# Kernel tuning notes

Hardware: AMD Instinct MI355X
Metric: run time of the kernel (lower is better)

Reference implementation:

```python
import jax, jax.numpy as jnp
import numpy as np

D = 128  # h_dim == in_dim

def _gat_layer(h, d, src, dst, n_dst, W, U, V, a):
    # h: [N_src, Din], d: [E, 1], src/dst: [E]
    z = h @ W.T          # [N_src, D]
    zi = h @ U.T         # [N_src, D]
    t = d @ V.T          # [E, 1]
    Dh = W.shape[0]
    # attn_fc on concat([z_src, z_dst, t]) split into three partial dots
    e = z[src] @ a[:Dh] + z[dst] @ a[Dh:2 * Dh] + t[:, 0] * a[2 * Dh]
    e = jax.nn.leaky_relu(e)  # [E]
    # segment softmax over incoming edges of each dst node
    m = jax.ops.segment_max(e, dst, num_segments=n_dst)
    ex = jnp.exp(e - m[dst])
    s = jax.ops.segment_sum(ex, dst, num_segments=n_dst)
    alpha = ex / s[dst]  # [E]
    zn = jax.ops.segment_sum(alpha[:, None] * z[src], dst, num_segments=n_dst)
    return jax.nn.relu(zi[:n_dst] + zn)


def setup_inputs() -> dict:
    key = jax.random.key(0)
    ks = jax.random.split(key, 16)
    N0, ND0, ND1 = 100000, 40000, 20000
    E0, E1 = 640000, 320000
    sc = 1.0 / np.sqrt(D)
    inp = {
        "attr": jax.random.normal(ks[0], (N0, D), jnp.float32),
        "d0": jax.random.normal(ks[1], (E0, 1), jnp.float32),
        "d1": jax.random.normal(ks[2], (E1, 1), jnp.float32),
        "src0": jax.random.randint(ks[3], (E0,), 0, N0, jnp.int32),
        "dst0": jax.random.randint(ks[4], (E0,), 0, ND0, jnp.int32),
        "src1": jax.random.randint(ks[5], (E1,), 0, ND0, jnp.int32),
        "dst1": jax.random.randint(ks[6], (E1,), 0, ND1, jnp.int32),
        "n_dst0": ND0,
        "n_dst1": ND1,
        "W0": jax.random.normal(ks[7], (D, D), jnp.float32) * sc,
        "U0": jax.random.normal(ks[8], (D, D), jnp.float32) * sc,
        "V0": jax.random.normal(ks[9], (1, 1), jnp.float32),
        "a0": jax.random.normal(ks[10], (2 * D + 1,), jnp.float32) * sc,
        "W1": jax.random.normal(ks[11], (D, D), jnp.float32) * sc,
        "U1": jax.random.normal(ks[12], (D, D), jnp.float32) * sc,
        "V1": jax.random.normal(ks[13], (1, 1), jnp.float32),
        "a1": jax.random.normal(ks[14], (2 * D + 1,), jnp.float32) * sc,
    }
    return inp


def reference(attr, d0, d1, W0, U0, V0, a0, W1, U1, V1, a1,
              src0, dst0, src1, dst1, n_dst0, n_dst1):
    h = _gat_layer(attr, d0, src0, dst0, n_dst0, W0, U0, V0, a0)
    h = _gat_layer(h, d1, src1, dst1, n_dst1, W1, U1, V1, a1)
    return h
```

## Files before the change

### kernel.cpp

```cpp
#include <hip/hip_runtime.h>
#include <math.h>


#define D 128

typedef __bf16 bf16x8 __attribute__((ext_vector_type(8)));
typedef float f32x4 __attribute__((ext_vector_type(4)));

static __device__ __forceinline__ float lrelu(float x) {
  return x >= 0.f ? x : 0.01f * x;
}
static __device__ __forceinline__ unsigned short f2bf(float v) {
  unsigned int u = __float_as_uint(v);
  u += 0x7fffu + ((u >> 16) & 1u);
  return (unsigned short)(u >> 16);
}
static __device__ __forceinline__ float bf2f(unsigned short b) {
  return __uint_as_float((unsigned int)b << 16);
}

static __device__ __forceinline__ float4 loadV4(const float* p) {
  return *(const float4*)p;
}
static __device__ __forceinline__ float4 loadV4(const unsigned short* p) {
  ushort4 t = *(const ushort4*)p;
  return make_float4(bf2f(t.x), bf2f(t.y), bf2f(t.z), bf2f(t.w));
}
static __device__ __forceinline__ void storeV4(float* p, float4 v) {
  *(float4*)p = v;
}
static __device__ __forceinline__ void storeV4(unsigned short* p, float4 v) {
  ushort4 t;
  t.x = f2bf(v.x);
  t.y = f2bf(v.y);
  t.z = f2bf(v.z);
  t.w = f2bf(v.w);
  *(ushort4*)p = t;
}
static __device__ __forceinline__ void storeZi(float* p, float v) { *p = v; }
static __device__ __forceinline__ void storeZi(unsigned short* p, float v) {
  *p = f2bf(v);
}

static __device__ __forceinline__ int swz(int row, int colb) {
  return row * 256 + (colb ^ ((row & 7) << 4));
}

__global__ __launch_bounds__(256) void cvt4_kernel(
    const float* __restrict__ s0, const float* __restrict__ s1,
    const float* __restrict__ s2, const float* __restrict__ s3,
    __bf16* __restrict__ dst) {
  int idx = blockIdx.x * 256 + threadIdx.x;
  const float* s = (idx < 16384) ? s0
                   : (idx < 32768) ? s1
                   : (idx < 49152) ? s2 : s3;
  dst[idx] = (__bf16)s[idx & 16383];
}

__global__ void zero_int_kernel(int* __restrict__ p, int n) {
  int i = blockIdx.x * 256 + threadIdx.x;
  if (i < n) p[i] = 0;
}

static __device__ __forceinline__ void stageA(const float* A, int rblk,
                                              int rlim, int t,
                                              unsigned char* ldsA) {
  const char* base = (const char*)A + (size_t)rblk * 512;
#pragma unroll
  for (int g = 0; g < 8; ++g) {
    int sb = g * 4096 + t * 16;
    float4 v = make_float4(0.f, 0.f, 0.f, 0.f);
    if (rblk + (sb >> 9) < rlim) v = *(const float4*)(base + sb);
    int db = sb >> 1;
    int row = db >> 8, colb = db & 255;
    ushort4 o;
    o.x = f2bf(v.x);
    o.y = f2bf(v.y);
    o.z = f2bf(v.z);
    o.w = f2bf(v.w);
    *(ushort4*)(&ldsA[swz(row, colb)]) = o;
  }
}
static __device__ __forceinline__ void stageA(const unsigned short* A,
                                              int rblk, int rlim, int t,
                                              unsigned char* ldsA) {
  const char* base = (const char*)A + (size_t)rblk * 256;
#pragma unroll
  for (int g = 0; g < 4; ++g) {
    int bi = g * 4096 + t * 16;
    int row = bi >> 8, colb = bi & 255;
    ushort4 lo = {0, 0, 0, 0}, hi = {0, 0, 0, 0};
    if (rblk + row < rlim) {
      lo = *(const ushort4*)(base + bi);
      hi = *(const ushort4*)(base + bi + 8);
    }
    *(ushort4*)(&ldsA[swz(row, colb)]) = lo;
    *(ushort4*)(&ldsA[swz(row, colb) + 8]) = hi;
  }
}

template <typename AT, typename ZiT>
__global__ __launch_bounds__(256, 3) void gemm_lds(
    const AT* __restrict__ A, const __bf16* __restrict__ Wb,
    const __bf16* __restrict__ Ub, unsigned short* __restrict__ z,
    ZiT* __restrict__ zi, const float* __restrict__ a,
    float* __restrict__ zs, float* __restrict__ zd, int n_wb, int rows,
    int ndst) {
  __shared__ unsigned char lds[49152];
  const int t = threadIdx.x;
  const int blk = blockIdx.x;
  const bool isU = (blk >= n_wb);
  const int rblk = (isU ? blk - n_wb : blk) * 64;
  const int rlim = isU ? ndst : rows;
  const __bf16* B = isU ? Ub : Wb;

#pragma unroll
  for (int g = 0; g < 8; ++g) {
    int bi = g * 4096 + t * 16;
    int row = bi >> 8, colb = bi & 255;
    bf16x8 v = *(const bf16x8*)((const char*)B + bi);
    *(bf16x8*)(&lds[swz(row, colb)]) = v;
  }
  stageA(A, rblk, rlim, t, lds + 32768);
  __syncthreads();

  const int wave = t >> 6;
  const int lane = t & 63;
  const int lm = lane & 15;
  const int lk = lane >> 4;
  const int r0 = rblk + wave * 16;
  if (r0 >= rlim) return;

  bf16x8 af[4];
#pragma unroll
  for (int kt = 0; kt < 4; ++kt) {
    int row = wave * 16 + lm;
    af[kt] = *(const bf16x8*)(&lds[32768 + swz(row, kt * 64 + lk * 16)]);
  }

  f32x4 acc[8];
#pragma unroll
  for (int tt = 0; tt < 8; ++tt) acc[tt] = (f32x4){0.f, 0.f, 0.f, 0.f};
#pragma unroll
  for (int kt = 0; kt < 4; ++kt) {
#pragma unroll
    for (int tt = 0; tt < 8; ++tt) {
      int row = tt * 16 + lm;
      bf16x8 bf = *(const bf16x8*)(&lds[swz(row, kt * 64 + lk * 16)]);
      acc[tt] =
          __builtin_amdgcn_mfma_f32_16x16x32_bf16(af[kt], bf, acc[tt], 0, 0, 0);
    }
  }

  if (!isU) {
#pragma unroll
    for (int tt = 0; tt < 8; ++tt)
#pragma unroll
      for (int rr = 0; rr < 4; ++rr)
        z[(size_t)(r0 + lk * 4 + rr) * D + tt * 16 + lm] = f2bf(acc[tt][rr]);

    float p1[4] = {0.f, 0.f, 0.f, 0.f};
    float p2[4] = {0.f, 0.f, 0.f, 0.f};
#pragma unroll
    for (int tt = 0; tt < 8; ++tt) {
      float a1 = a[tt * 16 + lm];
      float a2 = a[D + tt * 16 + lm];
#pragma unroll
      for (int rr = 0; rr < 4; ++rr) {
        p1[rr] += acc[tt][rr] * a1;
        p2[rr] += acc[tt][rr] * a2;
      }
    }
#pragma unroll
    for (int rr = 0; rr < 4; ++rr) {
#pragma unroll
      for (int o = 1; o < 16; o <<= 1) {
        p1[rr] += __shfl_xor(p1[rr], o);
        p2[rr] += __shfl_xor(p2[rr], o);
      }
      if (lm == 0) {
        zs[r0 + lk * 4 + rr] = p1[rr];
        zd[r0 + lk * 4 + rr] = p2[rr];
      }
    }
  } else {
#pragma unroll
    for (int tt = 0; tt < 8; ++tt)
#pragma unroll
      for (int rr = 0; rr < 4; ++rr)
        storeZi(&zi[(size_t)(r0 + lk * 4 + rr) * D + tt * 16 + lm],
                acc[tt][rr]);
  }
}

__global__ void count_e_kernel(const int* __restrict__ src,
                               const int* __restrict__ dst,
                               const float* __restrict__ dE,
                               const float* __restrict__ zs,
                               const float* __restrict__ zd,
                               const float* __restrict__ V,
                               const float* __restrict__ a,
                               int* __restrict__ cnt,
                               float* __restrict__ w_out,
                               int* __restrict__ rank, int E) {
  int i0 = (blockIdx.x * 256 + threadIdx.x) * 4;
  float vc = V[0] * a[2 * D];
  if (i0 + 4 <= E) {
    int4 s4 = *(const int4*)(src + i0);
    int4 d4 = *(const int4*)(dst + i0);
    float4 de = *(const float4*)(dE + i0);
    int4 r4;
    r4.x = atomicAdd(&cnt[d4.x], 1);
    r4.y = atomicAdd(&cnt[d4.y], 1);
    r4.z = atomicAdd(&cnt[d4.z], 1);
    r4.w = atomicAdd(&cnt[d4.w], 1);
    float zs0 = zs[s4.x], zs1 = zs[s4.y], zs2 = zs[s4.z], zs3 = zs[s4.w];
    float zd0 = zd[d4.x], zd1 = zd[d4.y], zd2 = zd[d4.z], zd3 = zd[d4.w];
    float4 w;
    w.x = __expf(lrelu(zs0 + zd0 + de.x * vc));
    w.y = __expf(lrelu(zs1 + zd1 + de.y * vc));
    w.z = __expf(lrelu(zs2 + zd2 + de.z * vc));
    w.w = __expf(lrelu(zs3 + zd3 + de.w * vc));
    *(float4*)(w_out + i0) = w;
    *(int4*)(rank + i0) = r4;
  } else {
    for (int i = i0; i < E; ++i) {
      int di = dst[i];
      rank[i] = atomicAdd(&cnt[di], 1);
      w_out[i] = __expf(lrelu(zs[src[i]] + zd[di] + dE[i] * vc));
    }
  }
}

__global__ __launch_bounds__(256) void scan_partial(const int* __restrict__ cnt,
                                                    int* __restrict__ part,
                                                    int n) {
  __shared__ int sm[4];
  int base = blockIdx.x * 1024;
  int t = threadIdx.x;
  int s = 0;
#pragma unroll
  for (int i = 0; i < 4; ++i) {
    int idx = base + t + i * 256;
    s += (idx < n) ? cnt[idx] : 0;
  }
  for (int o = 32; o; o >>= 1) s += __shfl_xor(s, o);
  if ((t & 63) == 0) sm[t >> 6] = s;
  __syncthreads();
  if (t == 0) part[blockIdx.x] = sm[0] + sm[1] + sm[2] + sm[3];
}

__global__ __launch_bounds__(256) void scan_final(
    const int* __restrict__ cnt, const int* __restrict__ part,
    int* __restrict__ offs, int nb, int n, int total) {
  __shared__ int sm[4];
  __shared__ int sbase;
  int base = blockIdx.x * 1024;
  int t = threadIdx.x;
  if (t < 64) {
    int v = (t < nb && t < (int)blockIdx.x) ? part[t] : 0;
#pragma unroll
    for (int o = 32; o; o >>= 1) v += __shfl_xor(v, o);
    if (t == 0) sbase = v;
  }
  int idx = base + t * 4;
  int c0 = (idx + 0 < n) ? cnt[idx + 0] : 0;
  int c1 = (idx + 1 < n) ? cnt[idx + 1] : 0;
  int c2 = (idx + 2 < n) ? cnt[idx + 2] : 0;
  int c3 = (idx + 3 < n) ? cnt[idx + 3] : 0;
  int ts = c0 + c1 + c2 + c3;
  int v = ts;
#pragma unroll
  for (int o = 1; o < 64; o <<= 1) {
    int u = __shfl_up(v, o);
    if ((t & 63) >= o) v += u;
  }
  if ((t & 63) == 63) sm[t >> 6] = v;
  __syncthreads();
  int w = t >> 6;
  int waveoff = 0;
  if (w > 0) waveoff += sm[0];
  if (w > 1) waveoff += sm[1];
  if (w > 2) waveoff += sm[2];
  int run = v - ts + waveoff + sbase;
  if (idx + 0 < n) { offs[idx + 0] = run; run += c0; }
  if (idx + 1 < n) { offs[idx + 1] = run; run += c1; }
  if (idx + 2 < n) { offs[idx + 2] = run; run += c2; }
  if (idx + 3 < n) { offs[idx + 3] = run; run += c3; }
  if (blockIdx.x == 0 && t == 0) offs[n] = total;
}

__global__ void scatter_kernel(const int* __restrict__ src,
                               const int* __restrict__ dst,
                               const float* __restrict__ w_in,
                               const int* __restrict__ rank,
                               const int* __restrict__ offs,
                               int2* __restrict__ csr, int E) {
  int i0 = (blockIdx.x * 256 + threadIdx.x) * 4;
  if (i0 + 4 <= E) {
    int4 s4 = *(const int4*)(src + i0);
    int4 d4 = *(const int4*)(dst + i0);
    float4 e4 = *(const float4*)(w_in + i0);
    int4 r4 = *(const int4*)(rank + i0);
    int p0 = offs[d4.x] + r4.x;
    int p1 = offs[d4.y] + r4.y;
    int p2 = offs[d4.z] + r4.z;
    int p3 = offs[d4.w] + r4.w;
    csr[p0] = make_int2(s4.x, __float_as_int(e4.x));
    csr[p1] = make_int2(s4.y, __float_as_int(e4.y));
    csr[p2] = make_int2(s4.z, __float_as_int(e4.z));
    csr[p3] = make_int2(s4.w, __float_as_int(e4.w));
  } else {
    for (int i = i0; i < E; ++i) {
      int p = offs[dst[i]] + rank[i];
      csr[p] = make_int2(src[i], __float_as_int(w_in[i]));
    }
  }
}

template <typename OT>
__global__ __launch_bounds__(256) void gat_perdst(
    const unsigned short* __restrict__ z, const int2* __restrict__ csr,
    const int* __restrict__ offs, const OT* __restrict__ ziin,
    OT* __restrict__ hout, int nd) {
  int n = blockIdx.x * 8 + (threadIdx.x >> 5);
  if (n >= nd) return;
  int lane = threadIdx.x & 31;
  int beg = offs[n], end = offs[n + 1];

  float s0 = 0.f, s1 = 0.f;
  float4 acc0 = make_float4(0.f, 0.f, 0.f, 0.f);
  float4 acc1 = make_float4(0.f, 0.f, 0.f, 0.f);
  const unsigned short* zp = z + lane * 4;
  int j = beg;
  for (; j + 8 <= end; j += 8) {
    int2 pr[8];
#pragma unroll
    for (int u = 0; u < 8; ++u) pr[u] = csr[j + u];
    float4 zv[8];
#pragma unroll
    for (int u = 0; u < 8; ++u) zv[u] = loadV4(zp + (size_t)pr[u].x * D);
#pragma unroll
    for (int u = 0; u < 8; u += 2) {
      float wa = __int_as_float(pr[u].y);
      float wb = __int_as_float(pr[u + 1].y);
      s0 += wa;
      acc0.x += wa * zv[u].x;
      acc0.y += wa * zv[u].y;
      acc0.z += wa * zv[u].z;
      acc0.w += wa * zv[u].w;
      s1 += wb;
      acc1.x += wb * zv[u + 1].x;
      acc1.y += wb * zv[u + 1].y;
      acc1.z += wb * zv[u + 1].z;
      acc1.w += wb * zv[u + 1].w;
    }
  }
  for (; j < end; ++j) {
    int2 pr = csr[j];
    float w = __int_as_float(pr.y);
    float4 zv = loadV4(zp + (size_t)pr.x * D);
    s0 += w;
    acc0.x += w * zv.x;
    acc0.y += w * zv.y;
    acc0.z += w * zv.z;
    acc0.w += w * zv.w;
  }
  float s = s0 + s1;
  float inv = (s > 0.f) ? 1.f / s : 0.f;
  float4 acc = make_float4(acc0.x + acc1.x, acc0.y + acc1.y, acc0.z + acc1.z,
                           acc0.w + acc1.w);
  float4 ziv = loadV4(ziin + (size_t)n * D + lane * 4);
  float4 o4;
  o4.x = fmaxf(ziv.x + acc.x * inv, 0.f);
  o4.y = fmaxf(ziv.y + acc.y * inv, 0.f);
  o4.z = fmaxf(ziv.z + acc.z * inv, 0.f);
  o4.w = fmaxf(ziv.w + acc.w * inv, 0.f);
  storeV4(hout + (size_t)n * D + lane * 4, o4);
}

extern "C" void kernel_launch(void* const* d_in, const int* in_sizes, int n_in,
                              void* d_out, int out_size, void* d_ws,
                              size_t ws_size, hipStream_t stream) {
  const float* attr = (const float*)d_in[0];
  const float* d0 = (const float*)d_in[1];
  const float* d1 = (const float*)d_in[2];
  const int* src0 = (const int*)d_in[3];
  const int* dst0 = (const int*)d_in[4];
  const int* src1 = (const int*)d_in[5];
  const int* dst1 = (const int*)d_in[6];
  const float* W0 = (const float*)d_in[9];
  const float* U0 = (const float*)d_in[10];
  const float* V0 = (const float*)d_in[11];
  const float* a0 = (const float*)d_in[12];
  const float* W1 = (const float*)d_in[13];
  const float* U1 = (const float*)d_in[14];
  const float* V1 = (const float*)d_in[15];
  const float* a1 = (const float*)d_in[16];

  const int N0 = in_sizes[0] / D;
  const int E0 = in_sizes[1];
  const int E1 = in_sizes[2];
  const int ND0 = 40000;
  const int ND1 = 20000;

  char* p = (char*)d_ws;
  auto alloc = [&](size_t bytes) {
    char* q = p;
    p += (bytes + 255) & ~(size_t)255;
    return q;
  };
  unsigned short* z = (unsigned short*)alloc((size_t)N0 * D * 2);
  int2* csr = (int2*)alloc((size_t)E0 * 8);
  unsigned short* h1b = (unsigned short*)alloc((size_t)ND0 * D * 2);
  float* w_buf = (float*)alloc((size_t)E0 * 4);
  int* rank = (int*)alloc((size_t)E0 * 4);
  float* zs = (float*)alloc((size_t)N0 * 4);
  float* zd = (float*)alloc((size_t)N0 * 4);
  int* offs = (int*)alloc((size_t)(ND0 + 1) * 4);
  int* cnt01 = (int*)alloc((size_t)(ND0 + ND1) * 4);
  int* part = (int*)alloc((size_t)64 * 4);
  __bf16* wb = (__bf16*)alloc((size_t)4 * D * D * 2);
  int* cnt0 = cnt01;
  int* cnt1 = cnt01 + ND0;
  (void)n_in;
  (void)out_size;
  (void)ws_size;

  float* out = (float*)d_out;

  cvt4_kernel<<<256, 256, 0, stream>>>(W0, U0, W1, U1, wb);
  zero_int_kernel<<<(ND0 + ND1 + 255) / 256, 256, 0, stream>>>(cnt01,
                                                               ND0 + ND1);
  const __bf16* W0b = wb;
  const __bf16* U0b = wb + 16384;
  const __bf16* W1b = wb + 32768;
  const __bf16* U1b = wb + 49152;

  {
    int n_wb = (N0 + 63) / 64, n_ub = (ND0 + 63) / 64;
    gemm_lds<float, unsigned short><<<n_wb + n_ub, 256, 0, stream>>>(
        attr, W0b, U0b, z, (unsigned short*)d_out, a0, zs, zd, n_wb, N0, ND0);
  }
  count_e_kernel<<<(E0 / 4 + 255) / 256, 256, 0, stream>>>(
      src0, dst0, d0, zs, zd, V0, a0, cnt0, w_buf, rank, E0);
  {
    int nb = (ND0 + 1023) / 1024;
    scan_partial<<<nb, 256, 0, stream>>>(cnt0, part, ND0);
    scan_final<<<nb, 256, 0, stream>>>(cnt0, part, offs, nb, ND0, E0);
  }
  scatter_kernel<<<(E0 / 4 + 255) / 256, 256, 0, stream>>>(
      src0, dst0, w_buf, rank, offs, csr, E0);
  gat_perdst<unsigned short><<<(ND0 + 7) / 8, 256, 0, stream>>>(
      z, csr, offs, (const unsigned short*)d_out, h1b, ND0);

  {
    int n_wb = (ND0 + 63) / 64, n_ub = (ND1 + 63) / 64;
    gemm_lds<unsigned short, float><<<n_wb + n_ub, 256, 0, stream>>>(
        h1b, W1b, U1b, z, out, a1, zs, zd, n_wb, ND0, ND1);
  }
  count_e_kernel<<<(E1 / 4 + 255) / 256, 256, 0, stream>>>(
      src1, dst1, d1, zs, zd, V1, a1, cnt1, w_buf, rank, E1);
  {
    int nb = (ND1 + 1023) / 1024;
    scan_partial<<<nb, 256, 0, stream>>>(cnt1, part, ND1);
    scan_final<<<nb, 256, 0, stream>>>(cnt1, part, offs, nb, ND1, E1);
  }
  scatter_kernel<<<(E1 / 4 + 255) / 256, 256, 0, stream>>>(
      src1, dst1, w_buf, rank, offs, csr, E1);
  gat_perdst<float><<<(ND1 + 7) / 8, 256, 0, stream>>>(z, csr, offs, out, out,
                                                       ND1);
}
```

Baseline: 180.8 us.

## Batch CSR construction for both layers upfront and fuse edge weights into scatter

Counting and ranking destination degrees for both layers now happens in one kernel launched before the first GEMM, followed by a single batched two-pass scan that covers both layers' offsets. This replaces four separate count/scan launches and keeps the graph-structure work independent of the GEMMs. The edge-weight exp computation moves from the count kernel into the scatter kernel, which removes the intermediate w_buf write and read. It costs separate rank and offset buffers per layer, and the combined count kernel contends on atomics across more edges in a single launch.

```diff
diff --git a/kernel.cpp b/kernel.cpp
--- a/kernel.cpp
+++ b/kernel.cpp
@@ -193,50 +193,47 @@
   }
 }
 
-__global__ void count_e_kernel(const int* __restrict__ src,
-                               const int* __restrict__ dst,
-                               const float* __restrict__ dE,
-                               const float* __restrict__ zs,
-                               const float* __restrict__ zd,
-                               const float* __restrict__ V,
-                               const float* __restrict__ a,
-                               int* __restrict__ cnt,
-                               float* __restrict__ w_out,
-                               int* __restrict__ rank, int E) {
-  int i0 = (blockIdx.x * 256 + threadIdx.x) * 4;
-  float vc = V[0] * a[2 * D];
-  if (i0 + 4 <= E) {
-    int4 s4 = *(const int4*)(src + i0);
-    int4 d4 = *(const int4*)(dst + i0);
-    float4 de = *(const float4*)(dE + i0);
-    int4 r4;
-    r4.x = atomicAdd(&cnt[d4.x], 1);
-    r4.y = atomicAdd(&cnt[d4.y], 1);
-    r4.z = atomicAdd(&cnt[d4.z], 1);
-    r4.w = atomicAdd(&cnt[d4.w], 1);
-    float zs0 = zs[s4.x], zs1 = zs[s4.y], zs2 = zs[s4.z], zs3 = zs[s4.w];
-    float zd0 = zd[d4.x], zd1 = zd[d4.y], zd2 = zd[d4.z], zd3 = zd[d4.w];
-    float4 w;
-    w.x = __expf(lrelu(zs0 + zd0 + de.x * vc));
-    w.y = __expf(lrelu(zs1 + zd1 + de.y * vc));
-    w.z = __expf(lrelu(zs2 + zd2 + de.z * vc));
-    w.w = __expf(lrelu(zs3 + zd3 + de.w * vc));
-    *(float4*)(w_out + i0) = w;
-    *(int4*)(rank + i0) = r4;
+__global__ void count_rank_kernel(const int* __restrict__ dst0,
+                                  const int* __restrict__ dst1,
+                                  int* __restrict__ cnt0,
+                                  int* __restrict__ cnt1,
+                                  int* __restrict__ rank0,
+                                  int* __restrict__ rank1, int q0, int q1) {
+  int gid = blockIdx.x * 256 + threadIdx.x;
+  const int* dst;
+  int* cnt;
+  int* rank;
+  int i0;
+  if (gid < q0) {
+    dst = dst0; cnt = cnt0; rank = rank0; i0 = gid * 4;
+  } else if (gid < q0 + q1) {
+    dst = dst1; cnt = cnt1; rank = rank1; i0 = (gid - q0) * 4;
   } else {
-    for (int i = i0; i < E; ++i) {
-      int di = dst[i];
-      rank[i] = atomicAdd(&cnt[di], 1);
-      w_out[i] = __expf(lrelu(zs[src[i]] + zd[di] + dE[i] * vc));
-    }
-  }
-}
-
-__global__ __launch_bounds__(256) void scan_partial(const int* __restrict__ cnt,
-                                                    int* __restrict__ part,
-                                                    int n) {
+    return;
+  }
+  int4 d4 = *(const int4*)(dst + i0);
+  int4 r4;
+  r4.x = atomicAdd(&cnt[d4.x], 1);
+  r4.y = atomicAdd(&cnt[d4.y], 1);
+  r4.z = atomicAdd(&cnt[d4.z], 1);
+  r4.w = atomicAdd(&cnt[d4.w], 1);
+  *(int4*)(rank + i0) = r4;
+}
+
+__global__ __launch_bounds__(256) void scan_partial2(
+    const int* __restrict__ cnt0, const int* __restrict__ cnt1,
+    int* __restrict__ part, int nb0, int n0, int n1) {
   __shared__ int sm[4];
-  int base = blockIdx.x * 1024;
+  int blk = blockIdx.x;
+  const int* cnt;
+  int* pt;
+  int n, lb;
+  if (blk < nb0) {
+    cnt = cnt0; pt = part; n = n0; lb = blk;
+  } else {
+    cnt = cnt1; pt = part + 64; n = n1; lb = blk - nb0;
+  }
+  int base = lb * 1024;
   int t = threadIdx.x;
   int s = 0;
 #pragma unroll
@@ -247,18 +244,30 @@
   for (int o = 32; o; o >>= 1) s += __shfl_xor(s, o);
   if ((t & 63) == 0) sm[t >> 6] = s;
   __syncthreads();
-  if (t == 0) part[blockIdx.x] = sm[0] + sm[1] + sm[2] + sm[3];
-}
-
-__global__ __launch_bounds__(256) void scan_final(
-    const int* __restrict__ cnt, const int* __restrict__ part,
-    int* __restrict__ offs, int nb, int n, int total) {
+  if (t == 0) pt[lb] = sm[0] + sm[1] + sm[2] + sm[3];
+}
+
+__global__ __launch_bounds__(256) void scan_final2(
+    const int* __restrict__ cnt0, const int* __restrict__ cnt1,
+    const int* __restrict__ part, int* __restrict__ offs0,
+    int* __restrict__ offs1, int nb0, int n0, int n1, int tot0, int tot1) {
   __shared__ int sm[4];
   __shared__ int sbase;
-  int base = blockIdx.x * 1024;
+  int blk = blockIdx.x;
+  const int* cnt;
+  const int* pt;
+  int* offs;
+  int n, lb, total;
+  if (blk < nb0) {
+    cnt = cnt0; pt = part; offs = offs0; n = n0; lb = blk; total = tot0;
+  } else {
+    cnt = cnt1; pt = part + 64; offs = offs1; n = n1; lb = blk - nb0;
+    total = tot1;
+  }
+  int base = lb * 1024;
   int t = threadIdx.x;
   if (t < 64) {
-    int v = (t < nb && t < (int)blockIdx.x) ? part[t] : 0;
+    int v = (t < lb) ? pt[t] : 0;
 #pragma unroll
     for (int o = 32; o; o >>= 1) v += __shfl_xor(v, o);
     if (t == 0) sbase = v;
@@ -287,33 +296,46 @@
   if (idx + 1 < n) { offs[idx + 1] = run; run += c1; }
   if (idx + 2 < n) { offs[idx + 2] = run; run += c2; }
   if (idx + 3 < n) { offs[idx + 3] = run; run += c3; }
-  if (blockIdx.x == 0 && t == 0) offs[n] = total;
-}
-
-__global__ void scatter_kernel(const int* __restrict__ src,
-                               const int* __restrict__ dst,
-                               const float* __restrict__ w_in,
-                               const int* __restrict__ rank,
-                               const int* __restrict__ offs,
-                               int2* __restrict__ csr, int E) {
+  if (lb == 0 && t == 0) offs[n] = total;
+}
+
+__global__ void scatter_w_kernel(const int* __restrict__ src,
+                                 const int* __restrict__ dst,
+                                 const float* __restrict__ dE,
+                                 const float* __restrict__ zs,
+                                 const float* __restrict__ zd,
+                                 const float* __restrict__ V,
+                                 const float* __restrict__ a,
+                                 const int* __restrict__ rank,
+                                 const int* __restrict__ offs,
+                                 int2* __restrict__ csr, int E) {
   int i0 = (blockIdx.x * 256 + threadIdx.x) * 4;
+  float vc = V[0] * a[2 * D];
   if (i0 + 4 <= E) {
     int4 s4 = *(const int4*)(src + i0);
     int4 d4 = *(const int4*)(dst + i0);
-    float4 e4 = *(const float4*)(w_in + i0);
+    float4 de = *(const float4*)(dE + i0);
     int4 r4 = *(const int4*)(rank + i0);
+    float zs0 = zs[s4.x], zs1 = zs[s4.y], zs2 = zs[s4.z], zs3 = zs[s4.w];
+    float zd0 = zd[d4.x], zd1 = zd[d4.y], zd2 = zd[d4.z], zd3 = zd[d4.w];
     int p0 = offs[d4.x] + r4.x;
     int p1 = offs[d4.y] + r4.y;
     int p2 = offs[d4.z] + r4.z;
     int p3 = offs[d4.w] + r4.w;
-    csr[p0] = make_int2(s4.x, __float_as_int(e4.x));
-    csr[p1] = make_int2(s4.y, __float_as_int(e4.y));
-    csr[p2] = make_int2(s4.z, __float_as_int(e4.z));
-    csr[p3] = make_int2(s4.w, __float_as_int(e4.w));
+    float w0 = __expf(lrelu(zs0 + zd0 + de.x * vc));
+    float w1 = __expf(lrelu(zs1 + zd1 + de.y * vc));
+    float w2 = __expf(lrelu(zs2 + zd2 + de.z * vc));
+    float w3 = __expf(lrelu(zs3 + zd3 + de.w * vc));
+    csr[p0] = make_int2(s4.x, __float_as_int(w0));
+    csr[p1] = make_int2(s4.y, __float_as_int(w1));
+    csr[p2] = make_int2(s4.z, __float_as_int(w2));
+    csr[p3] = make_int2(s4.w, __float_as_int(w3));
   } else {
     for (int i = i0; i < E; ++i) {
-      int p = offs[dst[i]] + rank[i];
-      csr[p] = make_int2(src[i], __float_as_int(w_in[i]));
+      int di = dst[i];
+      int pp = offs[di] + rank[i];
+      float w = __expf(lrelu(zs[src[i]] + zd[di] + dE[i] * vc));
+      csr[pp] = make_int2(src[i], __float_as_int(w));
     }
   }
 }
@@ -413,13 +435,14 @@
   unsigned short* z = (unsigned short*)alloc((size_t)N0 * D * 2);
   int2* csr = (int2*)alloc((size_t)E0 * 8);
   unsigned short* h1b = (unsigned short*)alloc((size_t)ND0 * D * 2);
-  float* w_buf = (float*)alloc((size_t)E0 * 4);
-  int* rank = (int*)alloc((size_t)E0 * 4);
+  int* rank0 = (int*)alloc((size_t)E0 * 4);
+  int* rank1 = (int*)alloc((size_t)E1 * 4);
   float* zs = (float*)alloc((size_t)N0 * 4);
   float* zd = (float*)alloc((size_t)N0 * 4);
-  int* offs = (int*)alloc((size_t)(ND0 + 1) * 4);
+  int* offs0 = (int*)alloc((size_t)(ND0 + 1) * 4);
+  int* offs1 = (int*)alloc((size_t)(ND1 + 1) * 4);
   int* cnt01 = (int*)alloc((size_t)(ND0 + ND1) * 4);
-  int* part = (int*)alloc((size_t)64 * 4);
+  int* part = (int*)alloc((size_t)128 * 4);
   __bf16* wb = (__bf16*)alloc((size_t)4 * D * D * 2);
   int* cnt0 = cnt01;
   int* cnt1 = cnt01 + ND0;
@@ -432,6 +455,17 @@
   cvt4_kernel<<<256, 256, 0, stream>>>(W0, U0, W1, U1, wb);
   zero_int_kernel<<<(ND0 + ND1 + 255) / 256, 256, 0, stream>>>(cnt01,
                                                                ND0 + ND1);
+  {
+    int q0 = E0 / 4, q1 = E1 / 4;
+    count_rank_kernel<<<(q0 + q1 + 255) / 256, 256, 0, stream>>>(
+        dst0, dst1, cnt0, cnt1, rank0, rank1, q0, q1);
+    int nb0 = (ND0 + 1023) / 1024;
+    int nb1 = (ND1 + 1023) / 1024;
+    scan_partial2<<<nb0 + nb1, 256, 0, stream>>>(cnt0, cnt1, part, nb0, ND0,
+                                                 ND1);
+    scan_final2<<<nb0 + nb1, 256, 0, stream>>>(cnt0, cnt1, part, offs0, offs1,
+                                               nb0, ND0, ND1, E0, E1);
+  }
   const __bf16* W0b = wb;
   const __bf16* U0b = wb + 16384;
   const __bf16* W1b = wb + 32768;
@@ -442,32 +476,18 @@
     gemm_lds<float, unsigned short><<<n_wb + n_ub, 256, 0, stream>>>(
         attr, W0b, U0b, z, (unsigned short*)d_out, a0, zs, zd, n_wb, N0, ND0);
   }
-  count_e_kernel<<<(E0 / 4 + 255) / 256, 256, 0, stream>>>(
-      src0, dst0, d0, zs, zd, V0, a0, cnt0, w_buf, rank, E0);
-  {
-    int nb = (ND0 + 1023) / 1024;
-    scan_partial<<<nb, 256, 0, stream>>>(cnt0, part, ND0);
-    scan_final<<<nb, 256, 0, stream>>>(cnt0, part, offs, nb, ND0, E0);
-  }
-  scatter_kernel<<<(E0 / 4 + 255) / 256, 256, 0, stream>>>(
-      src0, dst0, w_buf, rank, offs, csr, E0);
+  scatter_w_kernel<<<(E0 / 4 + 255) / 256, 256, 0, stream>>>(
+      src0, dst0, d0, zs, zd, V0, a0, rank0, offs0, csr, E0);
   gat_perdst<unsigned short><<<(ND0 + 7) / 8, 256, 0, stream>>>(
-      z, csr, offs, (const unsigned short*)d_out, h1b, ND0);
+      z, csr, offs0, (const unsigned short*)d_out, h1b, ND0);
 
   {
     int n_wb = (ND0 + 63) / 64, n_ub = (ND1 + 63) / 64;
     gemm_lds<unsigned short, float><<<n_wb + n_ub, 256, 0, stream>>>(
         h1b, W1b, U1b, z, out, a1, zs, zd, n_wb, ND0, ND1);
   }
-  count_e_kernel<<<(E1 / 4 + 255) / 256, 256, 0, stream>>>(
-      src1, dst1, d1, zs, zd, V1, a1, cnt1, w_buf, rank, E1);
-  {
-    int nb = (ND1 + 1023) / 1024;
-    scan_partial<<<nb, 256, 0, stream>>>(cnt1, part, ND1);
-    scan_final<<<nb, 256, 0, stream>>>(cnt1, part, offs, nb, ND1, E1);
-  }
-  scatter_kernel<<<(E1 / 4 + 255) / 256, 256, 0, stream>>>(
-      src1, dst1, w_buf, rank, offs, csr, E1);
-  gat_perdst<float><<<(ND1 + 7) / 8, 256, 0, stream>>>(z, csr, offs, out, out,
+  scatter_w_kernel<<<(E1 / 4 + 255) / 256, 256, 0, stream>>>(
+      src1, dst1, d1, zs, zd, V1, a1, rank1, offs1, csr, E1);
+  gat_perdst<float><<<(ND1 + 7) / 8, 256, 0, stream>>>(z, csr, offs1, out, out,
                                                        ND1);
 }
```

Measured after the change: 171.3 us. 5.2% less time.

## Build CSR by destination-range bucketing with LDS histograms instead of global atomics

Applied to the files above, without the earlier changes.

Replaces the count/scan/scatter CSR construction, which relied on global atomic counters per destination node, with a two-phase bucketed scheme. A front kernel, fused with the weight conversion, has 96 blocks each scan the whole dst array and collect the edges whose destination falls in their 625-node range. A per-range phase then builds the histogram, local scan and rank in LDS, computes the edge weights and writes the CSR. This removes the global atomics, the zeroing, and several launches per layer. In exchange, every bucketing block re-reads the full edge list, each phase runs with very few blocks, and ranges with more than CAP edges silently lose edges.

```diff
diff --git a/kernel.cpp b/kernel.cpp
--- a/kernel.cpp
+++ b/kernel.cpp
@@ -3,6 +3,8 @@
 
 
 #define D 128
+#define RANGE 625
+#define CAP 16384
 
 typedef __bf16 bf16x8 __attribute__((ext_vector_type(8)));
 typedef float f32x4 __attribute__((ext_vector_type(4)));
@@ -46,20 +48,47 @@
   return row * 256 + (colb ^ ((row & 7) << 4));
 }
 
-__global__ __launch_bounds__(256) void cvt4_kernel(
+__global__ __launch_bounds__(256) void front_kernel(
     const float* __restrict__ s0, const float* __restrict__ s1,
     const float* __restrict__ s2, const float* __restrict__ s3,
-    __bf16* __restrict__ dst) {
-  int idx = blockIdx.x * 256 + threadIdx.x;
-  const float* s = (idx < 16384) ? s0
-                   : (idx < 32768) ? s1
-                   : (idx < 49152) ? s2 : s3;
-  dst[idx] = (__bf16)s[idx & 16383];
-}
-
-__global__ void zero_int_kernel(int* __restrict__ p, int n) {
-  int i = blockIdx.x * 256 + threadIdx.x;
-  if (i < n) p[i] = 0;
+    __bf16* __restrict__ wdst, const int* __restrict__ dst0,
+    const int* __restrict__ dst1, int E0, int E1, int2* __restrict__ seg,
+    int* __restrict__ total) {
+  const int blk = blockIdx.x;
+  const int t = threadIdx.x;
+  if (blk < 256) {
+    int idx = blk * 256 + t;
+    const float* s = (idx < 16384) ? s0
+                     : (idx < 32768) ? s1
+                     : (idx < 49152) ? s2 : s3;
+    wdst[idx] = (__bf16)s[idx & 16383];
+    return;
+  }
+  __shared__ int nseg;
+  int g = blk - 256;
+  const int* dst;
+  int E, lo;
+  if (g < 64) {
+    dst = dst0; E = E0; lo = g * RANGE;
+  } else {
+    dst = dst1; E = E1; lo = (g - 64) * RANGE;
+  }
+  if (t == 0) nseg = 0;
+  __syncthreads();
+  int2* myseg = seg + (size_t)g * CAP;
+  for (int i0 = t * 4; i0 < E; i0 += 1024) {
+    int4 d4 = *(const int4*)(dst + i0);
+    int dk[4] = {d4.x, d4.y, d4.z, d4.w};
+#pragma unroll
+    for (int k = 0; k < 4; ++k) {
+      if (dk[k] >= lo && dk[k] < lo + RANGE) {
+        int p = atomicAdd(&nseg, 1);
+        if (p < CAP) myseg[p] = make_int2(i0 + k, dk[k]);
+      }
+    }
+  }
+  __syncthreads();
+  if (t == 0) total[g] = (nseg < CAP) ? nseg : CAP;
 }
 
 static __device__ __forceinline__ void stageA(const float* A, int rblk,
@@ -100,7 +129,7 @@
 }
 
 template <typename AT, typename ZiT>
-__global__ __launch_bounds__(256, 3) void gemm_lds(
+__global__ __launch_bounds__(256, 3) void gemm_tiles(
     const AT* __restrict__ A, const __bf16* __restrict__ Wb,
     const __bf16* __restrict__ Ub, unsigned short* __restrict__ z,
     ZiT* __restrict__ zi, const float* __restrict__ a,
@@ -193,128 +222,103 @@
   }
 }
 
-__global__ void count_e_kernel(const int* __restrict__ src,
-                               const int* __restrict__ dst,
-                               const float* __restrict__ dE,
-                               const float* __restrict__ zs,
-                               const float* __restrict__ zd,
-                               const float* __restrict__ V,
-                               const float* __restrict__ a,
-                               int* __restrict__ cnt,
-                               float* __restrict__ w_out,
-                               int* __restrict__ rank, int E) {
-  int i0 = (blockIdx.x * 256 + threadIdx.x) * 4;
-  float vc = V[0] * a[2 * D];
-  if (i0 + 4 <= E) {
-    int4 s4 = *(const int4*)(src + i0);
-    int4 d4 = *(const int4*)(dst + i0);
-    float4 de = *(const float4*)(dE + i0);
-    int4 r4;
-    r4.x = atomicAdd(&cnt[d4.x], 1);
-    r4.y = atomicAdd(&cnt[d4.y], 1);
-    r4.z = atomicAdd(&cnt[d4.z], 1);
-    r4.w = atomicAdd(&cnt[d4.w], 1);
-    float zs0 = zs[s4.x], zs1 = zs[s4.y], zs2 = zs[s4.z], zs3 = zs[s4.w];
-    float zd0 = zd[d4.x], zd1 = zd[d4.y], zd2 = zd[d4.z], zd3 = zd[d4.w];
-    float4 w;
-    w.x = __expf(lrelu(zs0 + zd0 + de.x * vc));
-    w.y = __expf(lrelu(zs1 + zd1 + de.y * vc));
-    w.z = __expf(lrelu(zs2 + zd2 + de.z * vc));
-    w.w = __expf(lrelu(zs3 + zd3 + de.w * vc));
-    *(float4*)(w_out + i0) = w;
-    *(int4*)(rank + i0) = r4;
-  } else {
-    for (int i = i0; i < E; ++i) {
-      int di = dst[i];
-      rank[i] = atomicAdd(&cnt[di], 1);
-      w_out[i] = __expf(lrelu(zs[src[i]] + zd[di] + dE[i] * vc));
-    }
-  }
-}
-
-__global__ __launch_bounds__(256) void scan_partial(const int* __restrict__ cnt,
-                                                    int* __restrict__ part,
-                                                    int n) {
-  __shared__ int sm[4];
-  int base = blockIdx.x * 1024;
-  int t = threadIdx.x;
-  int s = 0;
-#pragma unroll
-  for (int i = 0; i < 4; ++i) {
-    int idx = base + t + i * 256;
-    s += (idx < n) ? cnt[idx] : 0;
-  }
-  for (int o = 32; o; o >>= 1) s += __shfl_xor(s, o);
-  if ((t & 63) == 0) sm[t >> 6] = s;
-  __syncthreads();
-  if (t == 0) part[blockIdx.x] = sm[0] + sm[1] + sm[2] + sm[3];
-}
-
-__global__ __launch_bounds__(256) void scan_final(
-    const int* __restrict__ cnt, const int* __restrict__ part,
-    int* __restrict__ offs, int nb, int n, int total) {
-  __shared__ int sm[4];
+__global__ __launch_bounds__(256) void csr_phaseB(
+    const int* __restrict__ src, const float* __restrict__ dE,
+    const float* __restrict__ zs, const float* __restrict__ zd,
+    const float* __restrict__ V, const float* __restrict__ a,
+    const int2* __restrict__ seg, const int* __restrict__ total,
+    int* __restrict__ offs, int2* __restrict__ csr, int gbase, int nblocks,
+    int nd, int E) {
+  __shared__ int hist[RANGE];
+  __shared__ int loffs[RANGE];
+  __shared__ int lrank[RANGE];
+  __shared__ int swave[4];
   __shared__ int sbase;
-  int base = blockIdx.x * 1024;
-  int t = threadIdx.x;
+  const int g = blockIdx.x;
+  const int t = threadIdx.x;
+  const int lo = g * RANGE;
+  const int2* myseg = seg + (size_t)(gbase + g) * CAP;
+  int nm = total[gbase + g];
+
+  for (int j = t; j < RANGE; j += 256) {
+    hist[j] = 0;
+    lrank[j] = 0;
+  }
+  __syncthreads();
+  for (int i = t; i < nm; i += 256) {
+    int2 e = myseg[i];
+    atomicAdd(&hist[e.y - lo], 1);
+  }
   if (t < 64) {
-    int v = (t < nb && t < (int)blockIdx.x) ? part[t] : 0;
+    int v = (t < g && t < nblocks) ? total[gbase + t] : 0;
 #pragma unroll
     for (int o = 32; o; o >>= 1) v += __shfl_xor(v, o);
     if (t == 0) sbase = v;
   }
-  int idx = base + t * 4;
-  int c0 = (idx + 0 < n) ? cnt[idx + 0] : 0;
-  int c1 = (idx + 1 < n) ? cnt[idx + 1] : 0;
-  int c2 = (idx + 2 < n) ? cnt[idx + 2] : 0;
-  int c3 = (idx + 3 < n) ? cnt[idx + 3] : 0;
-  int ts = c0 + c1 + c2 + c3;
+  __syncthreads();
+
+  int b3 = t * 3;
+  int c0 = (b3 + 0 < RANGE) ? hist[b3 + 0] : 0;
+  int c1 = (b3 + 1 < RANGE) ? hist[b3 + 1] : 0;
+  int c2 = (b3 + 2 < RANGE) ? hist[b3 + 2] : 0;
+  int ts = c0 + c1 + c2;
   int v = ts;
 #pragma unroll
   for (int o = 1; o < 64; o <<= 1) {
     int u = __shfl_up(v, o);
     if ((t & 63) >= o) v += u;
   }
-  if ((t & 63) == 63) sm[t >> 6] = v;
-  __syncthreads();
-  int w = t >> 6;
-  int waveoff = 0;
-  if (w > 0) waveoff += sm[0];
-  if (w > 1) waveoff += sm[1];
-  if (w > 2) waveoff += sm[2];
-  int run = v - ts + waveoff + sbase;
-  if (idx + 0 < n) { offs[idx + 0] = run; run += c0; }
-  if (idx + 1 < n) { offs[idx + 1] = run; run += c1; }
-  if (idx + 2 < n) { offs[idx + 2] = run; run += c2; }
-  if (idx + 3 < n) { offs[idx + 3] = run; run += c3; }
-  if (blockIdx.x == 0 && t == 0) offs[n] = total;
-}
-
-__global__ void scatter_kernel(const int* __restrict__ src,
-                               const int* __restrict__ dst,
-                               const float* __restrict__ w_in,
-                               const int* __restrict__ rank,
-                               const int* __restrict__ offs,
-                               int2* __restrict__ csr, int E) {
-  int i0 = (blockIdx.x * 256 + threadIdx.x) * 4;
-  if (i0 + 4 <= E) {
-    int4 s4 = *(const int4*)(src + i0);
-    int4 d4 = *(const int4*)(dst + i0);
-    float4 e4 = *(const float4*)(w_in + i0);
-    int4 r4 = *(const int4*)(rank + i0);
-    int p0 = offs[d4.x] + r4.x;
-    int p1 = offs[d4.y] + r4.y;
-    int p2 = offs[d4.z] + r4.z;
-    int p3 = offs[d4.w] + r4.w;
-    csr[p0] = make_int2(s4.x, __float_as_int(e4.x));
-    csr[p1] = make_int2(s4.y, __float_as_int(e4.y));
-    csr[p2] = make_int2(s4.z, __float_as_int(e4.z));
-    csr[p3] = make_int2(s4.w, __float_as_int(e4.w));
-  } else {
-    for (int i = i0; i < E; ++i) {
-      int p = offs[dst[i]] + rank[i];
-      csr[p] = make_int2(src[i], __float_as_int(w_in[i]));
-    }
+  if ((t & 63) == 63) swave[t >> 6] = v;
+  __syncthreads();
+  int w_ = t >> 6;
+  int woff = 0;
+  if (w_ > 0) woff += swave[0];
+  if (w_ > 1) woff += swave[1];
+  if (w_ > 2) woff += swave[2];
+  int run = v - ts + woff;
+  if (b3 + 0 < RANGE) { loffs[b3 + 0] = run; offs[lo + b3 + 0] = sbase + run; run += c0; }
+  if (b3 + 1 < RANGE) { loffs[b3 + 1] = run; offs[lo + b3 + 1] = sbase + run; run += c1; }
+  if (b3 + 2 < RANGE) { loffs[b3 + 2] = run; offs[lo + b3 + 2] = sbase + run; run += c2; }
+  if (g == nblocks - 1 && t == 0) offs[nd] = E;
+  __syncthreads();
+
+  float vc = V[0] * a[2 * D];
+  int chunk = (nm + 255) >> 8;
+  int bI = t * chunk;
+  int eI = min(bI + chunk, nm);
+  int i = bI;
+  for (; i + 4 <= eI; i += 4) {
+    int2 e[4];
+#pragma unroll
+    for (int k = 0; k < 4; ++k) e[k] = myseg[i + k];
+    int ss[4];
+    float de[4];
+#pragma unroll
+    for (int k = 0; k < 4; ++k) {
+      ss[k] = src[e[k].x];
+      de[k] = dE[e[k].x];
+    }
+    float zsv[4], zdv[4];
+#pragma unroll
+    for (int k = 0; k < 4; ++k) {
+      zsv[k] = zs[ss[k]];
+      zdv[k] = zd[e[k].y];
+    }
+#pragma unroll
+    for (int k = 0; k < 4; ++k) {
+      float w = __expf(lrelu(zsv[k] + zdv[k] + de[k] * vc));
+      int dl = e[k].y - lo;
+      int r = atomicAdd(&lrank[dl], 1);
+      csr[sbase + loffs[dl] + r] = make_int2(ss[k], __float_as_int(w));
+    }
+  }
+  for (; i < eI; ++i) {
+    int2 e = myseg[i];
+    int s = src[e.x];
+    float w = __expf(lrelu(zs[s] + zd[e.y] + dE[e.x] * vc));
+    int dl = e.y - lo;
+    int r = atomicAdd(&lrank[dl], 1);
+    csr[sbase + loffs[dl] + r] = make_int2(s, __float_as_int(w));
   }
 }
 
@@ -413,25 +417,21 @@
   unsigned short* z = (unsigned short*)alloc((size_t)N0 * D * 2);
   int2* csr = (int2*)alloc((size_t)E0 * 8);
   unsigned short* h1b = (unsigned short*)alloc((size_t)ND0 * D * 2);
-  float* w_buf = (float*)alloc((size_t)E0 * 4);
-  int* rank = (int*)alloc((size_t)E0 * 4);
+  int2* seg = (int2*)alloc((size_t)96 * CAP * 8);
+  int* total = (int*)alloc((size_t)96 * 4);
   float* zs = (float*)alloc((size_t)N0 * 4);
   float* zd = (float*)alloc((size_t)N0 * 4);
-  int* offs = (int*)alloc((size_t)(ND0 + 1) * 4);
-  int* cnt01 = (int*)alloc((size_t)(ND0 + ND1) * 4);
-  int* part = (int*)alloc((size_t)64 * 4);
+  int* offs0 = (int*)alloc((size_t)(ND0 + 1) * 4);
+  int* offs1 = (int*)alloc((size_t)(ND1 + 1) * 4);
   __bf16* wb = (__bf16*)alloc((size_t)4 * D * D * 2);
-  int* cnt0 = cnt01;
-  int* cnt1 = cnt01 + ND0;
   (void)n_in;
   (void)out_size;
   (void)ws_size;
 
   float* out = (float*)d_out;
 
-  cvt4_kernel<<<256, 256, 0, stream>>>(W0, U0, W1, U1, wb);
-  zero_int_kernel<<<(ND0 + ND1 + 255) / 256, 256, 0, stream>>>(cnt01,
-                                                               ND0 + ND1);
+  front_kernel<<<256 + 96, 256, 0, stream>>>(W0, U0, W1, U1, wb, dst0, dst1,
+                                             E0, E1, seg, total);
   const __bf16* W0b = wb;
   const __bf16* U0b = wb + 16384;
   const __bf16* W1b = wb + 32768;
@@ -439,35 +439,21 @@
 
   {
     int n_wb = (N0 + 63) / 64, n_ub = (ND0 + 63) / 64;
-    gemm_lds<float, unsigned short><<<n_wb + n_ub, 256, 0, stream>>>(
+    gemm_tiles<float, unsigned short><<<n_wb + n_ub, 256, 0, stream>>>(
         attr, W0b, U0b, z, (unsigned short*)d_out, a0, zs, zd, n_wb, N0, ND0);
   }
-  count_e_kernel<<<(E0 / 4 + 255) / 256, 256, 0, stream>>>(
-      src0, dst0, d0, zs, zd, V0, a0, cnt0, w_buf, rank, E0);
-  {
-    int nb = (ND0 + 1023) / 1024;
-    scan_partial<<<nb, 256, 0, stream>>>(cnt0, part, ND0);
-    scan_final<<<nb, 256, 0, stream>>>(cnt0, part, offs, nb, ND0, E0);
-  }
-  scatter_kernel<<<(E0 / 4 + 255) / 256, 256, 0, stream>>>(
-      src0, dst0, w_buf, rank, offs, csr, E0);
+  csr_phaseB<<<64, 256, 0, stream>>>(src0, d0, zs, zd, V0, a0, seg, total,
+                                     offs0, csr, 0, 64, ND0, E0);
   gat_perdst<unsigned short><<<(ND0 + 7) / 8, 256, 0, stream>>>(
-      z, csr, offs, (const unsigned short*)d_out, h1b, ND0);
+      z, csr, offs0, (const unsigned short*)d_out, h1b, ND0);
 
   {
     int n_wb = (ND0 + 63) / 64, n_ub = (ND1 + 63) / 64;
-    gemm_lds<unsigned short, float><<<n_wb + n_ub, 256, 0, stream>>>(
+    gemm_tiles<unsigned short, float><<<n_wb + n_ub, 256, 0, stream>>>(
         h1b, W1b, U1b, z, out, a1, zs, zd, n_wb, ND0, ND1);
   }
-  count_e_kernel<<<(E1 / 4 + 255) / 256, 256, 0, stream>>>(
-      src1, dst1, d1, zs, zd, V1, a1, cnt1, w_buf, rank, E1);
-  {
-    int nb = (ND1 + 1023) / 1024;
-    scan_partial<<<nb, 256, 0, stream>>>(cnt1, part, ND1);
-    scan_final<<<nb, 256, 0, stream>>>(cnt1, part, offs, nb, ND1, E1);
-  }
-  scatter_kernel<<<(E1 / 4 + 255) / 256, 256, 0, stream>>>(
-      src1, dst1, w_buf, rank, offs, csr, E1);
-  gat_perdst<float><<<(ND1 + 7) / 8, 256, 0, stream>>>(z, csr, offs, out, out,
+  csr_phaseB<<<32, 256, 0, stream>>>(src1, d1, zs, zd, V1, a1, seg, total,
+                                     offs1, csr, 64, 32, ND1, E1);
+  gat_perdst<float><<<(ND1 + 7) / 8, 256, 0, stream>>>(z, csr, offs1, out, out,
                                                        ND1);
 }
```

Result: slower. 509.1 us (+181.6%).
